# Kernel tuning notes

Hardware: AMD Instinct MI355X
Metric: run time of the kernel (lower is better)

Reference implementation:

```python
import jax, jax.numpy as jnp
import numpy as np

B, S = 4, 1024
VD, TD, HD = 1024, 768, 2048
NH = 16
HDIM = HD // NH
SCALE = HDIM ** -0.5
THRESH = 2.0 / 3.0


def bitnet_linear(x, w, b):
    # BitNet b1.58 eval-mode: per-tensor abs-mean scale, clamp, ternarize, dense matmul
    scale = jnp.clip(jnp.mean(jnp.abs(w)), 1e-5, 1000.0)
    wn = jnp.clip(w / scale, -10.0, 10.0)
    q = jnp.where(wn > THRESH, 1.0, jnp.where(wn < -THRESH, -1.0, 0.0))
    return x @ (q * scale).T + b


def layernorm(x, g, b, eps=1e-5):
    mu = jnp.mean(x, axis=-1, keepdims=True)
    var = jnp.mean(jnp.square(x - mu), axis=-1, keepdims=True)
    return (x - mu) * jax.lax.rsqrt(var + eps) * g + b


def setup_inputs() -> dict:
    key = jax.random.key(0)
    ks = jax.random.split(key, 8)
    return {
        "vision_features": jax.random.normal(ks[0], (B, VD), jnp.float32),
        "text_features": jax.random.normal(ks[1], (B, S, TD), jnp.float32),
        "text_mask": jnp.ones((B, S), dtype=bool),
        "w_vision_proj": jax.random.normal(ks[2], (HD, VD), jnp.float32),
        "b_vision_proj": jnp.zeros((HD,), jnp.float32),
        "w_text_proj": jax.random.normal(ks[3], (HD, TD), jnp.float32),
        "b_text_proj": jnp.zeros((HD,), jnp.float32),
        "w_text_qkv": jax.random.normal(ks[4], (3 * HD, HD), jnp.float32),
        "b_text_qkv": jnp.zeros((3 * HD,), jnp.float32),
        "ln_text_g": jnp.ones((HD,), jnp.float32),
        "ln_text_b": jnp.zeros((HD,), jnp.float32),
        "w_out": jax.random.normal(ks[5], (HD, HD), jnp.float32),
        "b_out": jnp.zeros((HD,), jnp.float32),
        "ln_cross_g": jnp.ones((HD,), jnp.float32),
        "ln_cross_b": jnp.zeros((HD,), jnp.float32),
    }


def reference(vision_features, text_features, text_mask,
              w_vision_proj, b_vision_proj, w_text_proj, b_text_proj,
              w_text_qkv, b_text_qkv, ln_text_g, ln_text_b,
              w_out, b_out, ln_cross_g, ln_cross_b):
    # projections into shared hidden space (BitNet ternary linears)
    vp = bitnet_linear(vision_features, w_vision_proj, b_vision_proj)        # [B, HD]
    tp = bitnet_linear(text_features, w_text_proj, b_text_proj)              # [B, S, HD]

    # --- text self-attention (no rel-pos bias: the rel-pos branch raises and is swallowed) ---
    tn = layernorm(tp, ln_text_g, ln_text_b)
    qkv = bitnet_linear(tn, w_text_qkv, b_text_qkv)                          # [B, S, 3*HD]
    qkv = qkv.reshape(B, S, 3, NH, HDIM).transpose(2, 0, 3, 1, 4)            # [3, B, H, S, hd]
    tq, tk, tv = qkv[0], qkv[1], qkv[2]
    attn = jnp.einsum('bhqd,bhkd->bhqk', tq, tk) * SCALE                     # [B, H, S, S]
    attn = jnp.where(text_mask[:, None, None, :], attn, -1e9)
    attn = jax.nn.softmax(attn, axis=-1)
    text_self = jnp.einsum('bhqk,bhkd->bhqd', attn, tv)
    text_self = text_self.transpose(0, 2, 1, 3).reshape(B, S, HD)
    text_self = tp + text_self                                               # residual (dropout=id in eval)

    # --- image-to-text attention ---
    # original repeats the single vision query over seq then means the (identical)
    # outputs; mathematically equal to a single-query attention.
    vq = vp.reshape(B, NH, 1, HDIM)                                          # [B, H, 1, hd]
    tk2 = text_self.reshape(B, S, NH, HDIM).transpose(0, 2, 1, 3)            # [B, H, S, hd]
    i2t = jnp.einsum('bhqd,bhkd->bhqk', vq, tk2) * SCALE                     # [B, H, 1, S]
    i2t = jnp.where(text_mask[:, None, None, :], i2t, -1e9)
    i2t = jax.nn.softmax(i2t, axis=-1)
    i2t_out = jnp.einsum('bhqk,bhkd->bhqd', i2t, tk2).reshape(B, HD)         # [B, HD]

    # --- text-to-image attention (single kv "token" per head -> softmax over size-1 axis) ---
    tq2 = text_self.reshape(B, S, NH, HDIM).transpose(0, 2, 1, 3)            # [B, H, S, hd]
    vk = vp.reshape(B, NH, 1, HDIM)                                          # [B, H, 1, hd]
    t2i = jnp.einsum('bhqd,bhkd->bhqk', tq2, vk) * SCALE                     # [B, H, S, 1]
    t2i = jax.nn.softmax(t2i, axis=-1)                                       # all ones (size-1 axis)
    t2i_out = jnp.einsum('bhqk,bhkd->bhqd', t2i, vk)                         # [B, H, S, hd]
    t2i_out = t2i_out.transpose(0, 2, 1, 3).reshape(B, S, HD)

    # --- fusion: shared BitNet output projection + cross norm (inferred continuation) ---
    fused_vision = layernorm(vp + bitnet_linear(i2t_out, w_out, b_out), ln_cross_g, ln_cross_b)
    fused_text = layernorm(text_self + bitnet_linear(t2i_out, w_out, b_out), ln_cross_g, ln_cross_b)
    return fused_vision, fused_text
```

## Files before the change

kernel.cpp:

```cpp
#include <hip/hip_runtime.h>


typedef unsigned short u16;
typedef unsigned int   u32;
typedef __attribute__((ext_vector_type(4))) float f32x4;
typedef __attribute__((ext_vector_type(8))) short short8;
typedef _Float16 half8 __attribute__((ext_vector_type(8)));

__device__ __forceinline__ u16 f2h(float x) {
    _Float16 h = (_Float16)x;
    return __builtin_bit_cast(u16, h);
}
__device__ __forceinline__ f32x4 mfmah(short8 a, short8 b, f32x4 c) {
    return __builtin_amdgcn_mfma_f32_16x16x32_f16(
        __builtin_bit_cast(half8, a), __builtin_bit_cast(half8, b), c, 0, 0, 0);
}
__device__ __forceinline__ void gload16(const void* g, void* l) {
    __builtin_amdgcn_global_load_lds((const __attribute__((address_space(1))) u32*)g,
                                     (__attribute__((address_space(3))) u32*)l, 16, 0, 0);
}

__device__ __forceinline__ float blockReduceSum256(float v, float* red) {
#pragma unroll
    for (int o = 32; o; o >>= 1) v += __shfl_down(v, o);
    int lane = threadIdx.x & 63, w = threadIdx.x >> 6;
    __syncthreads();
    if (lane == 0) red[w] = v;
    __syncthreads();
    return red[0] + red[1] + red[2] + red[3];
}

__global__ __launch_bounds__(256) void k_absmean4(const float* __restrict__ w0, const float* __restrict__ w1,
                                                  const float* __restrict__ w2, const float* __restrict__ w3,
                                                  int n40, int n41, int n42, int n43,
                                                  double* __restrict__ part) {
    int slot = blockIdx.x >> 8, b = blockIdx.x & 255;
    const float* w = (slot == 0) ? w0 : (slot == 1) ? w1 : (slot == 2) ? w2 : w3;
    int n4 = (slot == 0) ? n40 : (slot == 1) ? n41 : (slot == 2) ? n42 : n43;
    const float4* w4 = (const float4*)w;
    double s = 0.0;
    for (int i = b * 256 + threadIdx.x; i < n4; i += 65536) {
        float4 v = w4[i];
        s += (double)fabsf(v.x) + (double)fabsf(v.y) + (double)fabsf(v.z) + (double)fabsf(v.w);
    }
#pragma unroll
    for (int o = 32; o; o >>= 1) s += __shfl_down(s, o);
    __shared__ double p4[4];
    int lane = threadIdx.x & 63, w_ = threadIdx.x >> 6;
    if (lane == 0) p4[w_] = s;
    __syncthreads();
    if (threadIdx.x == 0) part[slot * 256 + b] = p4[0] + p4[1] + p4[2] + p4[3];
}

__global__ void k_finalize(const double* __restrict__ part, float* __restrict__ scf) {
    int w = threadIdx.x >> 6, lane = threadIdx.x & 63;
    double s = 0.0;
    for (int j = lane; j < 256; j += 64) s += part[w * 256 + j];
#pragma unroll
    for (int o = 32; o; o >>= 1) s += __shfl_down(s, o);
    if (lane == 0) {
        const double ns[4] = {2097152.0, 1572864.0, 12582912.0, 4194304.0};
        float v = (float)(s / ns[w]);
        v = fminf(fmaxf(v, 1e-5f), 1000.0f);
        scf[w] = v;
    }
}

__global__ __launch_bounds__(256) void k_quant(const float* __restrict__ w, u32* __restrict__ qd,
                                               int n2, const float* __restrict__ scf, int slot) {
    float s = scf[slot];
    const float th = 2.0f / 3.0f;
    for (int i = blockIdx.x * blockDim.x + threadIdx.x; i < n2; i += gridDim.x * blockDim.x) {
        float2 v = ((const float2*)w)[i];
        float wn0 = v.x / s, wn1 = v.y / s;
        u32 q0 = (wn0 > th) ? 0x3C00u : ((wn0 < -th) ? 0xBC00u : 0u);
        u32 q1 = (wn1 > th) ? 0x3C00u : ((wn1 < -th) ? 0xBC00u : 0u);
        qd[i] = q0 | (q1 << 16);
    }
}

__global__ __launch_bounds__(256) void k_tofp16(const float* __restrict__ x, u32* __restrict__ xs, int n2) {
    for (int i = blockIdx.x * blockDim.x + threadIdx.x; i < n2; i += gridDim.x * blockDim.x) {
        float2 v = ((const float2*)x)[i];
        xs[i] = (u32)f2h(v.x) | (((u32)f2h(v.y)) << 16);
    }
}

__global__ __launch_bounds__(512, 2) void k_gemm(const u16* __restrict__ A, const u16* __restrict__ Bw,
                                                 int K, int N, int NB_N,
                                                 const float* __restrict__ scf, int slot,
                                                 const float* __restrict__ bias,
                                                 float* Cf, u16* Cp, int epi) {
    __shared__ __align__(16) u16 sA[4][4096];
    __shared__ __align__(16) u16 sB[4][8192];
    int t = threadIdx.x, lane = t & 63, w = t >> 6;
    int m0 = (blockIdx.x / NB_N) * 128;
    int n0 = (blockIdx.x % NB_N) * 256;
    int wm = (w >> 2) * 64, wn = (w & 3) * 64;
    f32x4 acc[4][4];
#pragma unroll
    for (int i = 0; i < 4; i++)
#pragma unroll
        for (int j = 0; j < 4; j++) acc[i][j] = (f32x4)(0.0f);

    const int NT = K >> 5;

    auto STAGE = [&](int sl, int kt) {
        int k0 = kt * 32;
        {
            int row = t & 127, kg = t >> 7;
            gload16(A + (size_t)(m0 + row) * K + (k0 + kg * 8),
                    sA[sl] + (size_t)(w * 64) * 8);
        }
#pragma unroll
        for (int i = 0; i < 2; i++) {
            int c = i * 512 + t;
            int col = c & 255, kg = c >> 8;
            gload16(Bw + (size_t)(n0 + col) * K + (k0 + kg * 8),
                    sB[sl] + (size_t)(i * 512 + w * 64) * 8);
        }
    };
    auto COMPUTE = [&](int sl) {
        short8 av[4], bv[4];
#pragma unroll
        for (int mi = 0; mi < 4; mi++)
            av[mi] = *(const short8*)(sA[sl] + (size_t)((lane >> 4) * 128 + wm + mi * 16 + (lane & 15)) * 8);
#pragma unroll
        for (int ni = 0; ni < 4; ni++)
            bv[ni] = *(const short8*)(sB[sl] + (size_t)((lane >> 4) * 256 + wn + ni * 16 + (lane & 15)) * 8);
        __builtin_amdgcn_s_setprio(1);
#pragma unroll
        for (int mi = 0; mi < 4; mi++)
#pragma unroll
            for (int ni = 0; ni < 4; ni++)
                acc[mi][ni] = mfmah(av[mi], bv[ni], acc[mi][ni]);
        __builtin_amdgcn_s_setprio(0);
    };

    STAGE(0, 0); STAGE(1, 1); STAGE(2, 2);
    for (int kt = 0; kt < NT - 2; ++kt) {
        asm volatile("s_waitcnt vmcnt(6)" ::: "memory");
        __builtin_amdgcn_s_barrier();
        if (kt + 3 < NT) STAGE((kt + 3) & 3, kt + 3);
        COMPUTE(kt & 3);
    }
    asm volatile("s_waitcnt vmcnt(3)" ::: "memory");
    __builtin_amdgcn_s_barrier();
    COMPUTE((NT - 2) & 3);
    asm volatile("s_waitcnt vmcnt(0)" ::: "memory");
    __builtin_amdgcn_s_barrier();
    COMPUTE((NT - 1) & 3);

    float s = scf[slot];
#pragma unroll
    for (int ni = 0; ni < 4; ni++) {
        int col = n0 + wn + ni * 16 + (lane & 15);
        float bv = bias[col];
#pragma unroll
        for (int mi = 0; mi < 4; mi++) {
            int rb = m0 + wm + mi * 16 + ((lane >> 4) << 2);
#pragma unroll
            for (int j = 0; j < 4; j++) {
                float y = acc[mi][ni][j] * s + bv;
                if (epi == 0) {
                    Cf[(size_t)(rb + j) * N + col] = y;
                } else {
                    Cp[(size_t)(rb + j) * N + col] = f2h(y);
                }
            }
        }
    }
}

__global__ __launch_bounds__(256) void k_vp(const float* __restrict__ vf, const float* __restrict__ w,
                                            const float* __restrict__ bias, const float* __restrict__ scf,
                                            float* __restrict__ vp) {
    __shared__ float xl[4096];
    int t = threadIdx.x;
#pragma unroll
    for (int i = 0; i < 16; i++) xl[t + i * 256] = vf[t + i * 256];
    __syncthreads();
    int lane = t & 63;
    int n = blockIdx.x * 4 + (t >> 6);
    float s = scf[0];
    const float th = 2.0f / 3.0f;
    float a0 = 0, a1 = 0, a2 = 0, a3 = 0;
    const float* wr = w + (size_t)n * 1024;
    for (int k = lane; k < 1024; k += 64) {
        float wn = wr[k] / s;
        float q = (wn > th) ? 1.0f : ((wn < -th) ? -1.0f : 0.0f);
        a0 += xl[k] * q; a1 += xl[1024 + k] * q; a2 += xl[2048 + k] * q; a3 += xl[3072 + k] * q;
    }
#pragma unroll
    for (int o = 32; o; o >>= 1) {
        a0 += __shfl_down(a0, o); a1 += __shfl_down(a1, o);
        a2 += __shfl_down(a2, o); a3 += __shfl_down(a3, o);
    }
    if (lane == 0) {
        float bv = bias[n];
        vp[n] = a0 * s + bv; vp[2048 + n] = a1 * s + bv;
        vp[4096 + n] = a2 * s + bv; vp[6144 + n] = a3 * s + bv;
    }
}

__global__ __launch_bounds__(256) void k_ln1(const float* __restrict__ x, const float* __restrict__ g,
                                             const float* __restrict__ b, u16* __restrict__ tn) {
    __shared__ float red[4];
    int r = blockIdx.x, t = threadIdx.x;
    const float* xr = x + (size_t)r * 2048;
    float v[8]; float s = 0;
#pragma unroll
    for (int i = 0; i < 8; i++) { v[i] = xr[t + i * 256]; s += v[i]; }
    s = blockReduceSum256(s, red);
    float mu = s * (1.0f / 2048.0f);
    float s2 = 0;
#pragma unroll
    for (int i = 0; i < 8; i++) { float d = v[i] - mu; s2 += d * d; }
    s2 = blockReduceSum256(s2, red);
    float rstd = 1.0f / sqrtf(s2 * (1.0f / 2048.0f) + 1e-5f);
#pragma unroll
    for (int i = 0; i < 8; i++) {
        int c = t + i * 256;
        float y = (v[i] - mu) * rstd * g[c] + b[c];
        tn[(size_t)r * 2048 + c] = f2h(y);
    }
}

__global__ __launch_bounds__(256) void k_attn(const u16* __restrict__ qkv, float* ts) {
    __shared__ __align__(16) u16 kp[8192];
    __shared__ __align__(16) u16 vt[128 * 72];
    int t = threadIdx.x, lane = t & 63, w = t >> 6;
    int bh = blockIdx.x >> 4, qb = blockIdx.x & 15;
    int b = bh >> 4, h = bh & 15;
    int rowbase = b * 1024;
    int q0 = qb * 64 + w * 16;
    u16* pl = kp + (size_t)w * 16 * 72;

    short8 qh[4];
    {
        int r = rowbase + q0 + (lane & 15);
        const u16* qp = qkv + (size_t)r * 6144 + h * 128 + (lane >> 4) * 8;
#pragma unroll
        for (int c4 = 0; c4 < 4; c4++) qh[c4] = *(const short8*)(qp + c4 * 32);
    }
    float m[4], ld[4];
#pragma unroll
    for (int j = 0; j < 4; j++) { m[j] = -1e30f; ld[j] = 0.0f; }
    f32x4 po[8];
#pragma unroll
    for (int nt = 0; nt < 8; nt++) po[nt] = (f32x4)(0.0f);
    const float SC = 0.08838834764831845f;

    for (int kt = 0; kt < 16; kt++) {
        __syncthreads();
#pragma unroll
        for (int i = 0; i < 4; i++) {
            int c = i * 256 + t;
            int sl = c & 63, dg = c >> 6;
            const u16* gk = qkv + (size_t)(rowbase + kt * 64 + sl) * 6144 + (2048 + h * 128 + dg * 8);
            gload16(gk, kp + (size_t)(i * 256 + w * 64) * 8);
        }
#pragma unroll
        for (int i = 0; i < 4; i++) {
            int c = i * 256 + t;
            int sl = c & 63, dg = c >> 6;
            const u16* gv = qkv + (size_t)(rowbase + kt * 64 + sl) * 6144 + (4096 + h * 128 + dg * 8);
            short8 vv = *(const short8*)gv;
#pragma unroll
            for (int j = 0; j < 8; j++) vt[(size_t)(dg * 8 + j) * 72 + sl] = (u16)vv[j];
        }
        __syncthreads();

        f32x4 sacc[4];
#pragma unroll
        for (int nt = 0; nt < 4; nt++) sacc[nt] = (f32x4)(0.0f);
#pragma unroll
        for (int c4 = 0; c4 < 4; c4++) {
            int kg = c4 * 4 + (lane >> 4);
#pragma unroll
            for (int nt = 0; nt < 4; nt++) {
                short8 kf = *(const short8*)(kp + (size_t)(kg * 64 + nt * 16 + (lane & 15)) * 8);
                sacc[nt] = mfmah(qh[c4], kf, sacc[nt]);
            }
        }
        float fsc[4], rs[4];
#pragma unroll
        for (int j = 0; j < 4; j++) {
            float mx = fmaxf(fmaxf(sacc[0][j], sacc[1][j]), fmaxf(sacc[2][j], sacc[3][j]));
            mx = fmaxf(mx, __shfl_xor(mx, 1));
            mx = fmaxf(mx, __shfl_xor(mx, 2));
            mx = fmaxf(mx, __shfl_xor(mx, 4));
            mx = fmaxf(mx, __shfl_xor(mx, 8));
            float mn = fmaxf(m[j], mx * SC);
            fsc[j] = expf(m[j] - mn);
            m[j] = mn; rs[j] = 0.0f;
        }
        __syncthreads();
#pragma unroll
        for (int nt = 0; nt < 4; nt++) {
#pragma unroll
            for (int j = 0; j < 4; j++) {
                float p = expf(sacc[nt][j] * SC - m[j]);
                rs[j] += p;
                pl[(size_t)((lane >> 4) * 4 + j) * 72 + nt * 16 + (lane & 15)] = f2h(p);
            }
        }
#pragma unroll
        for (int j = 0; j < 4; j++) {
            float r = rs[j];
            r += __shfl_xor(r, 1); r += __shfl_xor(r, 2);
            r += __shfl_xor(r, 4); r += __shfl_xor(r, 8);
            ld[j] = ld[j] * fsc[j] + r;
        }
#pragma unroll
        for (int nt = 0; nt < 8; nt++)
#pragma unroll
            for (int j = 0; j < 4; j++) po[nt][j] *= fsc[j];

#pragma unroll
        for (int kk2 = 0; kk2 < 2; kk2++) {
            short8 pa = *(const short8*)(pl + (size_t)(lane & 15) * 72 + kk2 * 32 + (lane >> 4) * 8);
#pragma unroll
            for (int nt = 0; nt < 8; nt++) {
                short8 vf = *(const short8*)(vt + (size_t)(nt * 16 + (lane & 15)) * 72 + kk2 * 32 + (lane >> 4) * 8);
                po[nt] = mfmah(pa, vf, po[nt]);
            }
        }
    }
#pragma unroll
    for (int nt = 0; nt < 8; nt++) {
        int d = nt * 16 + (lane & 15);
#pragma unroll
        for (int j = 0; j < 4; j++) {
            int r = rowbase + q0 + (lane >> 4) * 4 + j;
            size_t idx = (size_t)r * 2048 + h * 128 + d;
            ts[idx] = ts[idx] + po[nt][j] / ld[j];
        }
    }
}

__global__ __launch_bounds__(256) void k_i2t(const float* __restrict__ vp, const float* __restrict__ ts,
                                             float* __restrict__ io) {
    __shared__ float vq[128];
    __shared__ float sc[1024];
    __shared__ float red[4];
    __shared__ float part[256];
    int bh = blockIdx.x; int b = bh >> 4, h = bh & 15;
    int t = threadIdx.x, lane = t & 63, w = t >> 6;
    if (t < 128) vq[t] = vp[b * 2048 + h * 128 + t];
    __syncthreads();
    const float SC = 0.08838834764831845f;
    for (int s = w; s < 1024; s += 4) {
        const float* row = ts + (size_t)(b * 1024 + s) * 2048 + h * 128;
        float d = vq[lane] * row[lane] + vq[lane + 64] * row[lane + 64];
#pragma unroll
        for (int o = 32; o; o >>= 1) d += __shfl_down(d, o);
        if (lane == 0) sc[s] = d * SC;
    }
    __syncthreads();
    float mx = -1e30f;
    for (int s = t; s < 1024; s += 256) mx = fmaxf(mx, sc[s]);
#pragma unroll
    for (int o = 32; o; o >>= 1) mx = fmaxf(mx, __shfl_down(mx, o));
    if (lane == 0) red[w] = mx;
    __syncthreads();
    mx = fmaxf(fmaxf(red[0], red[1]), fmaxf(red[2], red[3]));
    __syncthreads();
    float sm = 0;
    for (int s = t; s < 1024; s += 256) { float p = expf(sc[s] - mx); sc[s] = p; sm += p; }
#pragma unroll
    for (int o = 32; o; o >>= 1) sm += __shfl_down(sm, o);
    if (lane == 0) red[w] = sm;
    __syncthreads();
    sm = red[0] + red[1] + red[2] + red[3];
    {
        int d = t & 127, sh = t >> 7;
        float acc = 0;
        const float* base = ts + (size_t)(b * 1024) * 2048 + h * 128 + d;
        for (int s = sh * 512; s < (sh + 1) * 512; s++) acc += sc[s] * base[(size_t)s * 2048];
        part[t] = acc;
    }
    __syncthreads();
    if (t < 128) io[b * 2048 + h * 128 + t] = (part[t] + part[128 + t]) / sm;
}

__global__ __launch_bounds__(256) void k_wout8(const float* __restrict__ i2t, const float* __restrict__ vp,
                                               const float* __restrict__ w, const float* __restrict__ bias,
                                               const float* __restrict__ scf, float* __restrict__ y8) {
    __shared__ float xl[8 * 2048];
    int t = threadIdx.x;
    for (int i = t; i < 16384; i += 256) {
        int rr = i >> 11, cc = i & 2047;
        xl[i] = (rr < 4) ? i2t[rr * 2048 + cc] : vp[(rr - 4) * 2048 + cc];
    }
    __syncthreads();
    int lane = t & 63;
    int n = blockIdx.x * 4 + (t >> 6);
    float s = scf[3];
    const float th = 2.0f / 3.0f;
    float a[8];
#pragma unroll
    for (int i = 0; i < 8; i++) a[i] = 0.0f;
    const float* wr = w + (size_t)n * 2048;
    for (int k = lane; k < 2048; k += 64) {
        float wn = wr[k] / s;
        float q = (wn > th) ? 1.0f : ((wn < -th) ? -1.0f : 0.0f);
#pragma unroll
        for (int i = 0; i < 8; i++) a[i] += xl[i * 2048 + k] * q;
    }
#pragma unroll
    for (int i = 0; i < 8; i++) {
#pragma unroll
        for (int o = 32; o; o >>= 1) a[i] += __shfl_down(a[i], o);
    }
    if (lane == 0) {
        float bv = bias[n];
#pragma unroll
        for (int i = 0; i < 8; i++) y8[i * 2048 + n] = a[i] * s + bv;
    }
}

__global__ __launch_bounds__(256) void k_fln(const float* __restrict__ xa, const float* __restrict__ y8,
                                             const float* __restrict__ g, const float* __restrict__ bb,
                                             float* __restrict__ out, int textmode) {
    __shared__ float red[4];
    int r = blockIdx.x, t = threadIdx.x;
    const float* a = xa + (size_t)r * 2048;
    const float* c = y8 + (size_t)(textmode ? (4 + (r >> 10)) : r) * 2048;
    float v[8]; float s = 0;
#pragma unroll
    for (int i = 0; i < 8; i++) { int cc = t + i * 256; v[i] = a[cc] + c[cc]; s += v[i]; }
    s = blockReduceSum256(s, red);
    float mu = s * (1.0f / 2048.0f);
    float s2 = 0;
#pragma unroll
    for (int i = 0; i < 8; i++) { float d = v[i] - mu; s2 += d * d; }
    s2 = blockReduceSum256(s2, red);
    float rstd = 1.0f / sqrtf(s2 * (1.0f / 2048.0f) + 1e-5f);
#pragma unroll
    for (int i = 0; i < 8; i++) {
        int cc = t + i * 256;
        out[(size_t)r * 2048 + cc] = (v[i] - mu) * rstd * g[cc] + bb[cc];
    }
}

extern "C" void kernel_launch(void* const* d_in, const int* in_sizes, int n_in,
                              void* d_out, int out_size, void* d_ws, size_t ws_size,
                              hipStream_t stream) {
    const float* vf    = (const float*)d_in[0];
    const float* tf    = (const float*)d_in[1];
    const float* w_vp  = (const float*)d_in[3];
    const float* b_vp  = (const float*)d_in[4];
    const float* w_tp  = (const float*)d_in[5];
    const float* b_tp  = (const float*)d_in[6];
    const float* w_qkv = (const float*)d_in[7];
    const float* b_qkv = (const float*)d_in[8];
    const float* lng   = (const float*)d_in[9];
    const float* lnb   = (const float*)d_in[10];
    const float* w_o   = (const float*)d_in[11];
    const float* b_o   = (const float*)d_in[12];
    const float* lcg   = (const float*)d_in[13];
    const float* lcb   = (const float*)d_in[14];
    float* out = (float*)d_out;
    char* ws = (char*)d_ws;

    constexpr size_t OFF_PART  = 0;
    constexpr size_t OFF_SCF   = 49152;
    constexpr size_t OFF_QDTP  = 65536;
    constexpr size_t OFF_QDQKV = 3276800;
    constexpr size_t OFF_XS    = 28442624;
    constexpr size_t OFF_TP    = 34734080;
    constexpr size_t OFF_TN    = 68288512;
    constexpr size_t OFF_QKV   = 85065728;
    constexpr size_t OFF_VP    = 135397376;
    constexpr size_t OFF_I2T   = 135430144;
    constexpr size_t OFF_Y8    = 135462912;

    double* part  = (double*)(ws + OFF_PART);
    float*  scf   = (float*)(ws + OFF_SCF);
    u16*   qd_tp  = (u16*)(ws + OFF_QDTP);
    u16*   qd_qkv = (u16*)(ws + OFF_QDQKV);
    u16*   xs     = (u16*)(ws + OFF_XS);
    float* tpb    = (float*)(ws + OFF_TP);
    u16*   tn     = (u16*)(ws + OFF_TN);
    u16*   qkvp   = (u16*)(ws + OFF_QKV);
    float* vpb    = (float*)(ws + OFF_VP);
    float* i2t    = (float*)(ws + OFF_I2T);
    float* y8     = (float*)(ws + OFF_Y8);

    k_absmean4<<<1024, 256, 0, stream>>>(w_vp, w_tp, w_qkv, w_o,
                                         2048 * 1024 / 4, 2048 * 768 / 4,
                                         6144 * 2048 / 4, 2048 * 2048 / 4, part);
    k_finalize<<<1, 256, 0, stream>>>(part, scf);

    k_quant<<<2048, 256, 0, stream>>>(w_tp,  (u32*)qd_tp,  2048 * 768  / 2, scf, 1);
    k_quant<<<4096, 256, 0, stream>>>(w_qkv, (u32*)qd_qkv, 6144 * 2048 / 2, scf, 2);
    k_tofp16<<<2048, 256, 0, stream>>>(tf, (u32*)xs, 4096 * 768 / 2);

    k_gemm<<<256, 512, 0, stream>>>(xs, qd_tp, 768, 2048, 8, scf, 1, b_tp, tpb, nullptr, 0);
    k_vp<<<512, 256, 0, stream>>>(vf, w_vp, b_vp, scf, vpb);

    k_ln1<<<4096, 256, 0, stream>>>(tpb, lng, lnb, tn);

    k_gemm<<<768, 512, 0, stream>>>(tn, qd_qkv, 2048, 6144, 24, scf, 2, b_qkv, nullptr, qkvp, 1);

    k_attn<<<1024, 256, 0, stream>>>(qkvp, tpb);

    k_i2t<<<64, 256, 0, stream>>>(vpb, tpb, i2t);

    k_wout8<<<512, 256, 0, stream>>>(i2t, vpb, w_o, b_o, scf, y8);

    k_fln<<<4, 256, 0, stream>>>(vpb, y8, lcg, lcb, out, 0);
    k_fln<<<4096, 256, 0, stream>>>(tpb, y8, lcg, lcb, out + 8192, 1);
    (void)in_sizes; (void)n_in; (void)out_size; (void)ws_size;
}
```

Measured before the change: 697.7 us.

## Enlarge GEMM tile to 256x256 with double-buffered 64-wide K phases

Replaces the 128x256 tile GEMM with a 256x256 tile that uses K=64 steps, two LDS buffers, and four quarter-phases per step. Loads for the next K step are split across the first two phases, with barriers around each MFMA burst. The goal is more reuse per loaded byte and less LDS/global traffic per FLOP. The cost is fewer blocks (128 and 384, below the 256-CU count for the first GEMM), more accumulator registers, and twice as many barriers.

```diff
diff --git a/kernel.cpp b/kernel.cpp
--- a/kernel.cpp
+++ b/kernel.cpp
@@ -86,70 +86,77 @@
     }
 }
 
-__global__ __launch_bounds__(512, 2) void k_gemm(const u16* __restrict__ A, const u16* __restrict__ Bw,
-                                                 int K, int N, int NB_N,
-                                                 const float* __restrict__ scf, int slot,
-                                                 const float* __restrict__ bias,
-                                                 float* Cf, u16* Cp, int epi) {
-    __shared__ __align__(16) u16 sA[4][4096];
-    __shared__ __align__(16) u16 sB[4][8192];
+#define QPHASE(KK, QM, SPART, DOVM)                                             \
+  {                                                                             \
+    short8 av[4], bv[4];                                                        \
+    _Pragma("unroll")                                                           \
+    for (int mi = 0; mi < 4; mi++)                                              \
+      av[mi] = *(const short8*)(sA[c] + (size_t)((((KK)*4 + (lane >> 4)) * 256) \
+                + wm + ((QM)*4 + mi) * 16 + (lane & 15)) * 8);                  \
+    _Pragma("unroll")                                                           \
+    for (int ni = 0; ni < 4; ni++)                                              \
+      bv[ni] = *(const short8*)(sB[c] + (size_t)((((KK)*4 + (lane >> 4)) * 256) \
+                + wn + ni * 16 + (lane & 15)) * 8);                             \
+    if ((SPART) >= 0 && kt + 1 < NT) STAGE_PART(c ^ 1, kt + 1, (SPART));        \
+    if ((DOVM) && kt + 1 < NT) asm volatile("s_waitcnt vmcnt(0)" ::: "memory"); \
+    __builtin_amdgcn_s_barrier();                                               \
+    asm volatile("s_waitcnt lgkmcnt(0)" ::: "memory");                          \
+    __builtin_amdgcn_sched_barrier(0);                                          \
+    __builtin_amdgcn_s_setprio(1);                                              \
+    _Pragma("unroll")                                                           \
+    for (int mi = 0; mi < 4; mi++)                                              \
+      _Pragma("unroll")                                                         \
+      for (int ni = 0; ni < 4; ni++)                                            \
+        acc[(QM)*4 + mi][ni] = mfmah(av[mi], bv[ni], acc[(QM)*4 + mi][ni]);     \
+    __builtin_amdgcn_s_setprio(0);                                              \
+    __builtin_amdgcn_s_barrier();                                               \
+  }
+
+__global__ __launch_bounds__(512, 2) void k_gemm256(const u16* __restrict__ A, const u16* __restrict__ Bw,
+                                                    int K, int N, int NB_N,
+                                                    const float* __restrict__ scf, int slot,
+                                                    const float* __restrict__ bias,
+                                                    float* Cf, u16* Cp, int epi) {
+    __shared__ __align__(16) u16 sA[2][16384];
+    __shared__ __align__(16) u16 sB[2][16384];
     int t = threadIdx.x, lane = t & 63, w = t >> 6;
-    int m0 = (blockIdx.x / NB_N) * 128;
+    int m0 = (blockIdx.x / NB_N) * 256;
     int n0 = (blockIdx.x % NB_N) * 256;
-    int wm = (w >> 2) * 64, wn = (w & 3) * 64;
-    f32x4 acc[4][4];
-#pragma unroll
-    for (int i = 0; i < 4; i++)
+    int wm = (w >> 2) * 128, wn = (w & 3) * 64;
+    const int NT = K >> 6;
+
+    f32x4 acc[8][4];
+#pragma unroll
+    for (int i = 0; i < 8; i++)
 #pragma unroll
         for (int j = 0; j < 4; j++) acc[i][j] = (f32x4)(0.0f);
 
-    const int NT = K >> 5;
-
-    auto STAGE = [&](int sl, int kt) {
-        int k0 = kt * 32;
-        {
-            int row = t & 127, kg = t >> 7;
+    auto STAGE_PART = [&](int buf, int kt2, int part) {
+        int k0 = kt2 << 6;
+#pragma unroll
+        for (int j = 0; j < 2; j++) {
+            int jj = part * 2 + j;
+            int cc = jj * 512 + t;
+            int row = cc & 255, kg = cc >> 8;
             gload16(A + (size_t)(m0 + row) * K + (k0 + kg * 8),
-                    sA[sl] + (size_t)(w * 64) * 8);
-        }
-#pragma unroll
-        for (int i = 0; i < 2; i++) {
-            int c = i * 512 + t;
-            int col = c & 255, kg = c >> 8;
-            gload16(Bw + (size_t)(n0 + col) * K + (k0 + kg * 8),
-                    sB[sl] + (size_t)(i * 512 + w * 64) * 8);
+                    sA[buf] + (size_t)(jj * 512 + w * 64) * 8);
+            gload16(Bw + (size_t)(n0 + row) * K + (k0 + kg * 8),
+                    sB[buf] + (size_t)(jj * 512 + w * 64) * 8);
         }
     };
-    auto COMPUTE = [&](int sl) {
-        short8 av[4], bv[4];
-#pragma unroll
-        for (int mi = 0; mi < 4; mi++)
-            av[mi] = *(const short8*)(sA[sl] + (size_t)((lane >> 4) * 128 + wm + mi * 16 + (lane & 15)) * 8);
-#pragma unroll
-        for (int ni = 0; ni < 4; ni++)
-            bv[ni] = *(const short8*)(sB[sl] + (size_t)((lane >> 4) * 256 + wn + ni * 16 + (lane & 15)) * 8);
-        __builtin_amdgcn_s_setprio(1);
-#pragma unroll
-        for (int mi = 0; mi < 4; mi++)
-#pragma unroll
-            for (int ni = 0; ni < 4; ni++)
-                acc[mi][ni] = mfmah(av[mi], bv[ni], acc[mi][ni]);
-        __builtin_amdgcn_s_setprio(0);
-    };
-
-    STAGE(0, 0); STAGE(1, 1); STAGE(2, 2);
-    for (int kt = 0; kt < NT - 2; ++kt) {
-        asm volatile("s_waitcnt vmcnt(6)" ::: "memory");
-        __builtin_amdgcn_s_barrier();
-        if (kt + 3 < NT) STAGE((kt + 3) & 3, kt + 3);
-        COMPUTE(kt & 3);
-    }
-    asm volatile("s_waitcnt vmcnt(3)" ::: "memory");
-    __builtin_amdgcn_s_barrier();
-    COMPUTE((NT - 2) & 3);
+
+    STAGE_PART(0, 0, 0);
+    STAGE_PART(0, 0, 1);
     asm volatile("s_waitcnt vmcnt(0)" ::: "memory");
     __builtin_amdgcn_s_barrier();
-    COMPUTE((NT - 1) & 3);
+
+    for (int kt = 0; kt < NT; kt++) {
+        int c = kt & 1;
+        QPHASE(0, 0, 0, 0)
+        QPHASE(0, 1, 1, 0)
+        QPHASE(1, 0, -1, 0)
+        QPHASE(1, 1, -1, 1)
+    }
 
     float s = scf[slot];
 #pragma unroll
@@ -157,7 +164,7 @@
         int col = n0 + wn + ni * 16 + (lane & 15);
         float bv = bias[col];
 #pragma unroll
-        for (int mi = 0; mi < 4; mi++) {
+        for (int mi = 0; mi < 8; mi++) {
             int rb = m0 + wm + mi * 16 + ((lane >> 4) << 2);
 #pragma unroll
             for (int j = 0; j < 4; j++) {
@@ -497,12 +504,12 @@
     k_quant<<<4096, 256, 0, stream>>>(w_qkv, (u32*)qd_qkv, 6144 * 2048 / 2, scf, 2);
     k_tofp16<<<2048, 256, 0, stream>>>(tf, (u32*)xs, 4096 * 768 / 2);
 
-    k_gemm<<<256, 512, 0, stream>>>(xs, qd_tp, 768, 2048, 8, scf, 1, b_tp, tpb, nullptr, 0);
+    k_gemm256<<<128, 512, 0, stream>>>(xs, qd_tp, 768, 2048, 8, scf, 1, b_tp, tpb, nullptr, 0);
     k_vp<<<512, 256, 0, stream>>>(vf, w_vp, b_vp, scf, vpb);
 
     k_ln1<<<4096, 256, 0, stream>>>(tpb, lng, lnb, tn);
 
-    k_gemm<<<768, 512, 0, stream>>>(tn, qd_qkv, 2048, 6144, 24, scf, 2, b_qkv, nullptr, qkvp, 1);
+    k_gemm256<<<384, 512, 0, stream>>>(tn, qd_qkv, 2048, 6144, 24, scf, 2, b_qkv, nullptr, qkvp, 1);
 
     k_attn<<<1024, 256, 0, stream>>>(qkvp, tpb);
 
```

After: 727.4 us. 1.04x slower.
